# Optimization experiments

Measured on AMD Instinct MI355X. Metric: run time of the kernel, lower is better.

Reference implementation:

```python
import jax, jax.numpy as jnp
import numpy as np

HIDDEN = 2048
NUM_HEADS = 16
HEAD_DIM = HIDDEN // NUM_HEADS  # 128
ROPE_BASE = 10000.0
BATCH = 2
SEQ = 2048


def _rope_cos_sin(seq_len, dim, base):
    inv_freq = 1.0 / (base ** (jnp.arange(0, dim, 2, dtype=jnp.float32) / dim))
    t = jnp.arange(seq_len, dtype=jnp.float32)
    freqs = jnp.outer(t, inv_freq)              # [S, dim/2]
    emb = jnp.concatenate([freqs, freqs], -1)   # [S, dim]
    return jnp.cos(emb), jnp.sin(emb)


def _rotate_half(x):
    d = x.shape[-1] // 2
    return jnp.concatenate([-x[..., d:], x[..., :d]], axis=-1)


def setup_inputs() -> dict:
    key = jax.random.key(0)
    ks = jax.random.split(key, 5)
    s = 1.0 / np.sqrt(HIDDEN)
    return {
        "hidden_states": jax.random.normal(ks[0], (BATCH, SEQ, HIDDEN), jnp.float32),
        "wq": jax.random.normal(ks[1], (HIDDEN, HIDDEN), jnp.float32) * s,
        "wk": jax.random.normal(ks[2], (HIDDEN, HIDDEN), jnp.float32) * s,
        "wv": jax.random.normal(ks[3], (HIDDEN, HIDDEN), jnp.float32) * s,
        "wo": jax.random.normal(ks[4], (HIDDEN, HIDDEN), jnp.float32) * s,
    }


def reference(hidden_states, wq, wk, wv, wo):
    b, s, _ = hidden_states.shape
    # Linear(bias=False): y = x @ W.T
    def proj(x, w):
        y = jnp.einsum('bsh,dh->bsd', x, w)
        return y.reshape(b, s, NUM_HEADS, HEAD_DIM).transpose(0, 2, 1, 3)  # [B,H,S,D]

    q = proj(hidden_states, wq)
    k = proj(hidden_states, wk)
    v = proj(hidden_states, wv)

    cos, sin = _rope_cos_sin(s, HEAD_DIM, ROPE_BASE)  # [S, D], broadcasts over B,H
    q = q * cos + _rotate_half(q) * sin
    k = k * cos + _rotate_half(k) * sin

    scale = 1.0 / np.sqrt(HEAD_DIM)
    scores = jnp.einsum('bhqd,bhkd->bhqk', q, k) * scale          # [B,H,S,S]
    attn = jax.nn.softmax(scores.astype(jnp.float32), axis=-1).astype(q.dtype)
    out = jnp.einsum('bhqk,bhkd->bhqd', attn, v)                  # [B,H,S,D]
    out = out.transpose(0, 2, 1, 3).reshape(b, s, HIDDEN)
    return jnp.einsum('bsh,dh->bsd', out, wo)
```

## Files before the change

kernel.cpp:

```cpp
#include <hip/hip_runtime.h>
#include <cstdint>
#include <cstddef>

typedef unsigned short u16;
typedef __attribute__((ext_vector_type(8))) __bf16 bf16x8;
typedef __attribute__((ext_vector_type(4))) float f32x4;
typedef __attribute__((ext_vector_type(8))) u16 u16x8;

#define GAS __attribute__((address_space(1)))
#define LAS __attribute__((address_space(3)))

static __device__ __forceinline__ u16 f2bf(float f) {
  uint32_t u = __builtin_bit_cast(uint32_t, f);
  u += 0x7fffu + ((u >> 16) & 1u);
  return (u16)(u >> 16);
}
static __device__ __forceinline__ float bf2f(u16 v) {
  uint32_t u = ((uint32_t)v) << 16;
  return __builtin_bit_cast(float, u);
}
static __device__ __forceinline__ bf16x8 ldf(const u16* p) {
  return __builtin_bit_cast(bf16x8, *reinterpret_cast<const u16x8*>(p));
}
static __device__ __forceinline__ void gld16(const void* g, void* l) {
  __builtin_amdgcn_global_load_lds((GAS unsigned int*)(uintptr_t)g,
                                   (LAS unsigned int*)l, 16, 0, 0);
}

__global__ __launch_bounds__(256) void castk(const float* __restrict__ s,
                                             u16* __restrict__ d, int n4) {
  int i = blockIdx.x * 256 + threadIdx.x;
  if (i < n4) {
    const float4 v = reinterpret_cast<const float4*>(s)[i];
    ushort4 o;
    o.x = f2bf(v.x); o.y = f2bf(v.y); o.z = f2bf(v.z); o.w = f2bf(v.w);
    reinterpret_cast<ushort4*>(d)[i] = o;
  }
}

__global__ __launch_bounds__(256, 2)
void gemm_bt(const u16* __restrict__ A, const u16* __restrict__ B,
             void* __restrict__ Cp, int M, int N, int K, int out_f32) {
  __shared__ alignas(16) u16 smA[2][128 * 32];
  __shared__ alignas(16) u16 smB[2][128 * 32];
  const int tid  = threadIdx.x;
  const int lane = tid & 63;
  const int w    = tid >> 6;
  const long m0 = (long)blockIdx.y * 128;
  const long n0 = (long)blockIdx.x * 128;
  const int wm = (w >> 1) * 64, wn = (w & 1) * 64;

  f32x4 acc[4][4] = {};

  const int lin0 = w * 64 + lane;
  const int lin1 = (4 + w) * 64 + lane;
  const int lrow0 = lin0 >> 2, lcol0 = (lin0 & 3) * 8;
  const int lrow1 = lin1 >> 2, lcol1 = (lin1 & 3) * 8;

  auto stage = [&](int buf, int k0) {
    gld16(A + (m0 + lrow0) * K + k0 + lcol0, &smA[buf][(0 * 4 + w) * 512]);
    gld16(B + (n0 + lrow0) * K + k0 + lcol0, &smB[buf][(0 * 4 + w) * 512]);
    gld16(A + (m0 + lrow1) * K + k0 + lcol1, &smA[buf][(1 * 4 + w) * 512]);
    gld16(B + (n0 + lrow1) * K + k0 + lcol1, &smB[buf][(1 * 4 + w) * 512]);
  };
  auto compute = [&](int buf) {
    const u16* As = smA[buf];
    const u16* Bs = smB[buf];
    const int k8 = (lane >> 4) * 8;
    bf16x8 af[4], bfr[4];
#pragma unroll
    for (int t = 0; t < 4; ++t) {
      af[t]  = ldf(As + (wm + t * 16 + (lane & 15)) * 32 + k8);
      bfr[t] = ldf(Bs + (wn + t * 16 + (lane & 15)) * 32 + k8);
    }
#pragma unroll
    for (int i = 0; i < 4; ++i)
#pragma unroll
      for (int j = 0; j < 4; ++j)
        acc[i][j] = __builtin_amdgcn_mfma_f32_16x16x32_bf16(af[i], bfr[j], acc[i][j], 0, 0, 0);
  };

  stage(0, 0);
  __syncthreads();
  const int NT = K >> 5;
  for (int t = 0; t < NT; ++t) {
    if (t + 1 < NT) stage((t + 1) & 1, (t + 1) << 5);
    compute(t & 1);
    __syncthreads();
  }

#pragma unroll
  for (int i = 0; i < 4; ++i)
#pragma unroll
    for (int j = 0; j < 4; ++j)
#pragma unroll
      for (int r = 0; r < 4; ++r) {
        long row = m0 + wm + i * 16 + (lane >> 4) * 4 + r;
        long col = n0 + wn + j * 16 + (lane & 15);
        if (out_f32) ((float*)Cp)[row * N + col] = acc[i][j][r];
        else         ((u16*)Cp)[row * N + col]   = f2bf(acc[i][j][r]);
      }
}

__global__ __launch_bounds__(256) void rope_q(u16* __restrict__ Q) {
  const int m = blockIdx.x;
  const int pos = m & 2047;
  const int t = threadIdx.x;
  const int j = t & 63;
  const float invf = exp2f(-(float)j * 0.20762050593046014f);
  float sn, cs;
  sincosf((float)pos * invf, &sn, &cs);
  const float sc = 0.08838834764831845f;
#pragma unroll
  for (int h = t >> 6; h < 16; h += 4) {
    u16* p = Q + (size_t)m * 2048 + h * 128;
    float a = bf2f(p[j]), b = bf2f(p[j + 64]);
    p[j]      = f2bf((a * cs - b * sn) * sc);
    p[j + 64] = f2bf((b * cs + a * sn) * sc);
  }
}

__global__ __launch_bounds__(256) void rope_k(const u16* __restrict__ Kt, u16* __restrict__ Kb) {
  const int m = blockIdx.x;
  const int pos = m & 2047;
  const int bb = m >> 11;
  const int kb = pos >> 6;
  const int key = pos & 63;
  const int t = threadIdx.x;
  const int j = t & 63;
  const float invf = exp2f(-(float)j * 0.20762050593046014f);
  float sn, cs;
  sincosf((float)pos * invf, &sn, &cs);
  const int sw = (key & 7) << 3;
#pragma unroll
  for (int h = t >> 6; h < 16; h += 4) {
    const u16* p = Kt + (size_t)m * 2048 + h * 128;
    float a = bf2f(p[j]), b = bf2f(p[j + 64]);
    u16* dst = Kb + ((size_t)(bb * 16 + h) * 32 + kb) * 8192 + key * 128;
    dst[j ^ sw]        = f2bf(a * cs - b * sn);
    dst[(j + 64) ^ sw] = f2bf(b * cs + a * sn);
  }
}

__global__ __launch_bounds__(256) void transpose_v(const u16* __restrict__ Vt, u16* __restrict__ Vb) {
  __shared__ u16 sm[64][130];
  const int kb = blockIdx.x, bh = blockIdx.y;
  const int bb = bh >> 4, h = bh & 15;
  const int t = threadIdx.x;
#pragma unroll
  for (int r = 0; r < 4; ++r) {
    int c = r * 256 + t;
    int key = c >> 4, d0 = (c & 15) * 8;
    const u16* src = Vt + (size_t)(bb * 2048 + kb * 64 + key) * 2048 + h * 128 + d0;
    u16x8 v = *reinterpret_cast<const u16x8*>(src);
#pragma unroll
    for (int i = 0; i < 8; ++i) sm[key][d0 + i] = v[i];
  }
  __syncthreads();
  u16* dst = Vb + ((size_t)bh * 32 + kb) * 8192;
#pragma unroll
  for (int r = 0; r < 4; ++r) {
    int c = r * 256 + t;
    int key0 = (c & 7) * 8, d = c >> 3;
    u16x8 v;
#pragma unroll
    for (int i = 0; i < 8; ++i) v[i] = sm[key0 + i][d];
    *reinterpret_cast<u16x8*>(dst + d * 64 + (key0 ^ ((d & 7) << 3))) = v;
  }
}

__global__ __launch_bounds__(256, 2)
void flash_attn(const u16* __restrict__ Q, const u16* __restrict__ Kb,
                const u16* __restrict__ Vb, u16* __restrict__ O) {
  __shared__ alignas(16) u16 smK[64 * 128];
  __shared__ alignas(16) u16 smV[128 * 64];
  __shared__ alignas(16) u16 smP[4][16 * 64];

  const int f = blockIdx.x;
  const int bh = (f & 7) * 4 + (f >> 8);
  const int qb = (f >> 3) & 31;
  const int bb = bh >> 4, h = bh & 15;
  const int lane = threadIdx.x & 63, w = threadIdx.x >> 6;

  const int qrow = bb * 2048 + qb * 64 + w * 16 + (lane & 15);
  const u16* qp = Q + (size_t)qrow * 2048 + h * 128 + ((lane >> 4) * 8);
  bf16x8 qf[4];
#pragma unroll
  for (int kk = 0; kk < 4; ++kk) qf[kk] = ldf(qp + kk * 32);

  f32x4 oacc[8] = {};
  float mr[4] = {-__builtin_inff(), -__builtin_inff(), -__builtin_inff(), -__builtin_inff()};
  float lr[4] = {0.f, 0.f, 0.f, 0.f};

  const u16* kbase = Kb + (size_t)bh * 32 * 8192;
  const u16* vbase = Vb + (size_t)bh * 32 * 8192;

  for (int kb = 0; kb < 32; ++kb) {
    __syncthreads();
#pragma unroll
    for (int j = 0; j < 4; ++j) {
      int off = (j * 4 + w) * 512;
      gld16(kbase + (size_t)kb * 8192 + off + lane * 8, &smK[off]);
      gld16(vbase + (size_t)kb * 8192 + off + lane * 8, &smV[off]);
    }
    __syncthreads();

    f32x4 sacc[4] = {};
#pragma unroll
    for (int nt = 0; nt < 4; ++nt) {
      const int key = nt * 16 + (lane & 15);
      const int sw = (key & 7) << 3;
#pragma unroll
      for (int kk = 0; kk < 4; ++kk) {
        const int d = kk * 32 + (lane >> 4) * 8;
        bf16x8 kf = ldf(&smK[key * 128 + (d ^ sw)]);
        sacc[nt] = __builtin_amdgcn_mfma_f32_16x16x32_bf16(qf[kk], kf, sacc[nt], 0, 0, 0);
      }
    }

    float nm[4], fac[4];
#pragma unroll
    for (int r = 0; r < 4; ++r) {
      float mx = fmaxf(fmaxf(sacc[0][r], sacc[1][r]), fmaxf(sacc[2][r], sacc[3][r]));
#pragma unroll
      for (int o = 1; o < 16; o <<= 1) mx = fmaxf(mx, __shfl_xor(mx, o));
      nm[r] = fmaxf(mr[r], mx);
      fac[r] = exp2f((mr[r] - nm[r]) * 1.4426950408889634f);
      mr[r] = nm[r];
    }
#pragma unroll
    for (int nt = 0; nt < 4; ++nt)
#pragma unroll
      for (int r = 0; r < 4; ++r)
        sacc[nt][r] = exp2f((sacc[nt][r] - nm[r]) * 1.4426950408889634f);
#pragma unroll
    for (int r = 0; r < 4; ++r) {
      float s = (sacc[0][r] + sacc[1][r]) + (sacc[2][r] + sacc[3][r]);
#pragma unroll
      for (int o = 1; o < 16; o <<= 1) s += __shfl_xor(s, o);
      lr[r] = lr[r] * fac[r] + s;
    }
#pragma unroll
    for (int t = 0; t < 8; ++t)
#pragma unroll
      for (int r = 0; r < 4; ++r) oacc[t][r] *= fac[r];

    u16* pw = smP[w];
#pragma unroll
    for (int r = 0; r < 4; ++r) {
      const int row = (lane >> 4) * 4 + r;
      const int sw = (row & 7) << 3;
#pragma unroll
      for (int nt = 0; nt < 4; ++nt) {
        const int col = nt * 16 + (lane & 15);
        pw[row * 64 + (col ^ sw)] = f2bf(sacc[nt][r]);
      }
    }

#pragma unroll
    for (int kk2 = 0; kk2 < 2; ++kk2) {
      const int k0 = kk2 * 32 + (lane >> 4) * 8;
      const int prow = lane & 15;
      bf16x8 pf = ldf(&pw[prow * 64 + (k0 ^ ((prow & 7) << 3))]);
#pragma unroll
      for (int t = 0; t < 8; ++t) {
        const int d = t * 16 + (lane & 15);
        bf16x8 vf = ldf(&smV[d * 64 + (k0 ^ ((d & 7) << 3))]);
        oacc[t] = __builtin_amdgcn_mfma_f32_16x16x32_bf16(pf, vf, oacc[t], 0, 0, 0);
      }
    }
  }

#pragma unroll
  for (int r = 0; r < 4; ++r) lr[r] = 1.0f / lr[r];
  const int orow0 = bb * 2048 + qb * 64 + w * 16;
#pragma unroll
  for (int t = 0; t < 8; ++t)
#pragma unroll
    for (int r = 0; r < 4; ++r) {
      const int row = orow0 + (lane >> 4) * 4 + r;
      const int d = t * 16 + (lane & 15);
      O[(size_t)row * 2048 + h * 128 + d] = f2bf(oacc[t][r] * lr[r]);
    }
}

extern "C" void kernel_launch(void* const* d_in, const int* in_sizes, int n_in,
                              void* d_out, int out_size, void* d_ws, size_t ws_size,
                              hipStream_t stream) {
  const float* X  = (const float*)d_in[0];
  const float* Wq = (const float*)d_in[1];
  const float* Wk = (const float*)d_in[2];
  const float* Wv = (const float*)d_in[3];
  const float* Wo = (const float*)d_in[4];
  float* out = (float*)d_out;
  char* ws = (char*)d_ws;
  const size_t MB = 1u << 20;
  u16* Xb   = (u16*)(ws + 0   * MB);
  u16* Qb   = (u16*)(ws + 16  * MB);
  u16* Ktmp = (u16*)(ws + 32  * MB);
  u16* Vtmp = (u16*)(ws + 48  * MB);
  u16* Vblk = (u16*)(ws + 64  * MB);
  u16* Wqb  = (u16*)(ws + 80  * MB);
  u16* Wkb  = (u16*)(ws + 88  * MB);
  u16* Wvb  = (u16*)(ws + 96  * MB);
  u16* Wob  = (u16*)(ws + 104 * MB);
  u16* Kblk = Xb;
  u16* Ob   = Ktmp;

  castk<<<8192, 256, 0, stream>>>(X,  Xb,  2097152);
  castk<<<4096, 256, 0, stream>>>(Wq, Wqb, 1048576);
  castk<<<4096, 256, 0, stream>>>(Wk, Wkb, 1048576);
  castk<<<4096, 256, 0, stream>>>(Wv, Wvb, 1048576);
  castk<<<4096, 256, 0, stream>>>(Wo, Wob, 1048576);

  gemm_bt<<<dim3(16, 32), 256, 0, stream>>>(Xb, Wqb, Qb,   4096, 2048, 2048, 0);
  gemm_bt<<<dim3(16, 32), 256, 0, stream>>>(Xb, Wkb, Ktmp, 4096, 2048, 2048, 0);
  gemm_bt<<<dim3(16, 32), 256, 0, stream>>>(Xb, Wvb, Vtmp, 4096, 2048, 2048, 0);

  rope_q<<<4096, 256, 0, stream>>>(Qb);
  rope_k<<<4096, 256, 0, stream>>>(Ktmp, Kblk);
  transpose_v<<<dim3(32, 32), 256, 0, stream>>>(Vtmp, Vblk);

  flash_attn<<<1024, 256, 0, stream>>>(Qb, Kblk, Vblk, Ob);

  gemm_bt<<<dim3(16, 32), 256, 0, stream>>>(Ob, Wob, out, 4096, 2048, 2048, 1);
}
```

Measured before the change: 530.5 us.

## Fuse QKV projections into one 256x256-tile GEMM with pipelined LDS staging

The three Q/K/V projections become one GEMM over a concatenated weight, writing a row-interleaved QKV buffer. The old 128x128 GEMM is replaced by a 512-thread kernel with 256x256 tiles, K-step 64 split into halves, manual barriers and vmcnt waits, an XCD-aware block remap and s_setprio around MFMA bursts. Flash attention also raises wave priority around its MFMA loops. The aim is more data reuse per tile and fewer launches. The cost is that the output GEMM runs only 128 workgroups, which may underfill the GPU.

```diff
diff --git a/kernel.cpp b/kernel.cpp
--- a/kernel.cpp
+++ b/kernel.cpp
@@ -26,6 +26,7 @@
   __builtin_amdgcn_global_load_lds((GAS unsigned int*)(uintptr_t)g,
                                    (LAS unsigned int*)l, 16, 0, 0);
 }
+#define MFMA __builtin_amdgcn_mfma_f32_16x16x32_bf16
 
 __global__ __launch_bounds__(256) void castk(const float* __restrict__ s,
                                              u16* __restrict__ d, int n4) {
@@ -38,71 +39,139 @@
   }
 }
 
-__global__ __launch_bounds__(256, 2)
-void gemm_bt(const u16* __restrict__ A, const u16* __restrict__ B,
-             void* __restrict__ Cp, int M, int N, int K, int out_f32) {
-  __shared__ alignas(16) u16 smA[2][128 * 32];
-  __shared__ alignas(16) u16 smB[2][128 * 32];
-  const int tid  = threadIdx.x;
-  const int lane = tid & 63;
-  const int w    = tid >> 6;
-  const long m0 = (long)blockIdx.y * 128;
-  const long n0 = (long)blockIdx.x * 128;
-  const int wm = (w >> 1) * 64, wn = (w & 1) * 64;
-
-  f32x4 acc[4][4] = {};
-
-  const int lin0 = w * 64 + lane;
-  const int lin1 = (4 + w) * 64 + lane;
-  const int lrow0 = lin0 >> 2, lcol0 = (lin0 & 3) * 8;
-  const int lrow1 = lin1 >> 2, lcol1 = (lin1 & 3) * 8;
-
-  auto stage = [&](int buf, int k0) {
-    gld16(A + (m0 + lrow0) * K + k0 + lcol0, &smA[buf][(0 * 4 + w) * 512]);
-    gld16(B + (n0 + lrow0) * K + k0 + lcol0, &smB[buf][(0 * 4 + w) * 512]);
-    gld16(A + (m0 + lrow1) * K + k0 + lcol1, &smA[buf][(1 * 4 + w) * 512]);
-    gld16(B + (n0 + lrow1) * K + k0 + lcol1, &smB[buf][(1 * 4 + w) * 512]);
+__global__ __launch_bounds__(512, 2)
+void gemm256(const u16* __restrict__ A, const u16* __restrict__ B,
+             void* __restrict__ Cp, int M, int N, int K, int out_f32, int nbx) {
+  __shared__ alignas(16) u16 sm[8][8192];
+  const int tid = threadIdx.x;
+  const int lane = tid & 63, w = tid >> 6;
+  const int wm = w >> 2, wn = w & 3;
+  const int lo = lane & 15, hi8 = (lane >> 4) << 3;
+
+  const int nwg = gridDim.x;
+  const int id = blockIdx.x;
+  const int idp = (id & 7) * (nwg >> 3) + (id >> 3);
+  const long m0 = (long)(idp / nbx) * 256;
+  const long n0 = (long)(idp % nbx) * 256;
+
+  const int srow = w * 16 + (lane >> 2);
+  const int scol = (lane & 3) * 8;
+  const u16* pA0 = A + (size_t)(m0 + srow) * K + scol;
+  const u16* pA1 = A + (size_t)(m0 + 128 + srow) * K + scol;
+  const u16* pB0 = B + (size_t)(n0 + srow) * K + scol;
+  const u16* pB1 = B + (size_t)(n0 + 128 + srow) * K + scol;
+  const int ldso = w * 512;
+
+  auto stA = [&](int slot, int half, int k0) {
+    u16* d = sm[(slot << 2) | half];
+    gld16(pA0 + k0 + half * 32, d + ldso);
+    gld16(pA1 + k0 + half * 32, d + 4096 + ldso);
   };
-  auto compute = [&](int buf) {
-    const u16* As = smA[buf];
-    const u16* Bs = smB[buf];
-    const int k8 = (lane >> 4) * 8;
-    bf16x8 af[4], bfr[4];
-#pragma unroll
-    for (int t = 0; t < 4; ++t) {
-      af[t]  = ldf(As + (wm + t * 16 + (lane & 15)) * 32 + k8);
-      bfr[t] = ldf(Bs + (wn + t * 16 + (lane & 15)) * 32 + k8);
-    }
-#pragma unroll
-    for (int i = 0; i < 4; ++i)
-#pragma unroll
-      for (int j = 0; j < 4; ++j)
-        acc[i][j] = __builtin_amdgcn_mfma_f32_16x16x32_bf16(af[i], bfr[j], acc[i][j], 0, 0, 0);
+  auto stB = [&](int slot, int half, int k0) {
+    u16* d = sm[(slot << 2) | 2 | half];
+    gld16(pB0 + k0 + half * 32, d + ldso);
+    gld16(pB1 + k0 + half * 32, d + 4096 + ldso);
   };
 
-  stage(0, 0);
-  __syncthreads();
-  const int NT = K >> 5;
-  for (int t = 0; t < NT; ++t) {
-    if (t + 1 < NT) stage((t + 1) & 1, (t + 1) << 5);
-    compute(t & 1);
-    __syncthreads();
-  }
-
-#pragma unroll
-  for (int i = 0; i < 4; ++i)
-#pragma unroll
-    for (int j = 0; j < 4; ++j)
-#pragma unroll
-      for (int r = 0; r < 4; ++r) {
-        long row = m0 + wm + i * 16 + (lane >> 4) * 4 + r;
-        long col = n0 + wn + j * 16 + (lane & 15);
-        if (out_f32) ((float*)Cp)[row * N + col] = acc[i][j][r];
-        else         ((u16*)Cp)[row * N + col]   = f2bf(acc[i][j][r]);
+  const int aoff = (wm * 128 + lo) * 32 + hi8;
+  const int boff = (wn * 64 + lo) * 32 + hi8;
+
+  f32x4 acc[8][4] = {};
+
+  stA(0, 0, 0); stB(0, 0, 0); stA(0, 1, 0); stB(0, 1, 0);
+  asm volatile("s_waitcnt vmcnt(4)" ::: "memory");
+  __builtin_amdgcn_s_barrier();
+
+  const int NT = K >> 6;
+  for (int kt = 0; kt < NT; ++kt) {
+    const int s = kt & 1, so = s ^ 1;
+    const int kn = (kt + 1 < NT) ? ((kt + 1) << 6) : 0;
+    const u16* sA0 = sm[(s << 2) | 0];
+    const u16* sA1 = sm[(s << 2) | 1];
+    const u16* sB0 = sm[(s << 2) | 2];
+    const u16* sB1 = sm[(s << 2) | 3];
+
+    bf16x8 af[8], b0, b1;
+    b0 = ldf(sB0 + boff);
+    b1 = ldf(sB0 + boff + 512);
+#pragma unroll
+    for (int mf = 0; mf < 8; ++mf) af[mf] = ldf(sA0 + aoff + mf * 512);
+    stA(so, 0, kn);
+    __builtin_amdgcn_s_barrier();
+    asm volatile("s_waitcnt lgkmcnt(0)" ::: "memory");
+    __builtin_amdgcn_s_setprio(1);
+#pragma unroll
+    for (int mf = 0; mf < 8; ++mf) {
+      acc[mf][0] = MFMA(af[mf], b0, acc[mf][0], 0, 0, 0);
+      acc[mf][1] = MFMA(af[mf], b1, acc[mf][1], 0, 0, 0);
+    }
+    __builtin_amdgcn_s_setprio(0);
+    __builtin_amdgcn_s_barrier();
+    b0 = ldf(sB0 + boff + 1024);
+    b1 = ldf(sB0 + boff + 1536);
+    stB(so, 0, kn);
+    __builtin_amdgcn_s_barrier();
+    asm volatile("s_waitcnt lgkmcnt(0)" ::: "memory");
+    __builtin_amdgcn_s_setprio(1);
+#pragma unroll
+    for (int mf = 0; mf < 8; ++mf) {
+      acc[mf][2] = MFMA(af[mf], b0, acc[mf][2], 0, 0, 0);
+      acc[mf][3] = MFMA(af[mf], b1, acc[mf][3], 0, 0, 0);
+    }
+    __builtin_amdgcn_s_setprio(0);
+    asm volatile("s_waitcnt vmcnt(4)" ::: "memory");
+    __builtin_amdgcn_s_barrier();
+    b0 = ldf(sB1 + boff);
+    b1 = ldf(sB1 + boff + 512);
+#pragma unroll
+    for (int mf = 0; mf < 8; ++mf) af[mf] = ldf(sA1 + aoff + mf * 512);
+    stA(so, 1, kn);
+    __builtin_amdgcn_s_barrier();
+    asm volatile("s_waitcnt lgkmcnt(0)" ::: "memory");
+    __builtin_amdgcn_s_setprio(1);
+#pragma unroll
+    for (int mf = 0; mf < 8; ++mf) {
+      acc[mf][0] = MFMA(af[mf], b0, acc[mf][0], 0, 0, 0);
+      acc[mf][1] = MFMA(af[mf], b1, acc[mf][1], 0, 0, 0);
+    }
+    __builtin_amdgcn_s_setprio(0);
+    __builtin_amdgcn_s_barrier();
+    b0 = ldf(sB1 + boff + 1024);
+    b1 = ldf(sB1 + boff + 1536);
+    stB(so, 1, kn);
+    __builtin_amdgcn_s_barrier();
+    asm volatile("s_waitcnt lgkmcnt(0)" ::: "memory");
+    __builtin_amdgcn_s_setprio(1);
+#pragma unroll
+    for (int mf = 0; mf < 8; ++mf) {
+      acc[mf][2] = MFMA(af[mf], b0, acc[mf][2], 0, 0, 0);
+      acc[mf][3] = MFMA(af[mf], b1, acc[mf][3], 0, 0, 0);
+    }
+    __builtin_amdgcn_s_setprio(0);
+    asm volatile("s_waitcnt vmcnt(4)" ::: "memory");
+    __builtin_amdgcn_s_barrier();
+  }
+  asm volatile("s_waitcnt vmcnt(0)" ::: "memory");
+
+#pragma unroll
+  for (int mf = 0; mf < 8; ++mf)
+#pragma unroll
+    for (int nf = 0; nf < 4; ++nf) {
+      const long row = m0 + wm * 128 + mf * 16 + (lane >> 4) * 4;
+      const long col = n0 + wn * 64 + nf * 16 + lo;
+      if (out_f32) {
+        float* C = (float*)Cp;
+#pragma unroll
+        for (int r = 0; r < 4; ++r) C[(row + r) * N + col] = acc[mf][nf][r];
+      } else {
+        u16* C = (u16*)Cp;
+#pragma unroll
+        for (int r = 0; r < 4; ++r) C[(row + r) * N + col] = f2bf(acc[mf][nf][r]);
       }
-}
-
-__global__ __launch_bounds__(256) void rope_q(u16* __restrict__ Q) {
+    }
+}
+
+__global__ __launch_bounds__(256) void rope_q(u16* __restrict__ QKV) {
   const int m = blockIdx.x;
   const int pos = m & 2047;
   const int t = threadIdx.x;
@@ -113,14 +182,14 @@
   const float sc = 0.08838834764831845f;
 #pragma unroll
   for (int h = t >> 6; h < 16; h += 4) {
-    u16* p = Q + (size_t)m * 2048 + h * 128;
+    u16* p = QKV + (size_t)m * 6144 + h * 128;
     float a = bf2f(p[j]), b = bf2f(p[j + 64]);
     p[j]      = f2bf((a * cs - b * sn) * sc);
     p[j + 64] = f2bf((b * cs + a * sn) * sc);
   }
 }
 
-__global__ __launch_bounds__(256) void rope_k(const u16* __restrict__ Kt, u16* __restrict__ Kb) {
+__global__ __launch_bounds__(256) void rope_k(const u16* __restrict__ QKV, u16* __restrict__ Kb) {
   const int m = blockIdx.x;
   const int pos = m & 2047;
   const int bb = m >> 11;
@@ -134,7 +203,7 @@
   const int sw = (key & 7) << 3;
 #pragma unroll
   for (int h = t >> 6; h < 16; h += 4) {
-    const u16* p = Kt + (size_t)m * 2048 + h * 128;
+    const u16* p = QKV + (size_t)m * 6144 + 2048 + h * 128;
     float a = bf2f(p[j]), b = bf2f(p[j + 64]);
     u16* dst = Kb + ((size_t)(bb * 16 + h) * 32 + kb) * 8192 + key * 128;
     dst[j ^ sw]        = f2bf(a * cs - b * sn);
@@ -142,8 +211,8 @@
   }
 }
 
-__global__ __launch_bounds__(256) void transpose_v(const u16* __restrict__ Vt, u16* __restrict__ Vb) {
-  __shared__ u16 sm[64][130];
+__global__ __launch_bounds__(256) void transpose_v(const u16* __restrict__ QKV, u16* __restrict__ Vb) {
+  __shared__ u16 smv[64][130];
   const int kb = blockIdx.x, bh = blockIdx.y;
   const int bb = bh >> 4, h = bh & 15;
   const int t = threadIdx.x;
@@ -151,10 +220,10 @@
   for (int r = 0; r < 4; ++r) {
     int c = r * 256 + t;
     int key = c >> 4, d0 = (c & 15) * 8;
-    const u16* src = Vt + (size_t)(bb * 2048 + kb * 64 + key) * 2048 + h * 128 + d0;
+    const u16* src = QKV + (size_t)(bb * 2048 + kb * 64 + key) * 6144 + 4096 + h * 128 + d0;
     u16x8 v = *reinterpret_cast<const u16x8*>(src);
 #pragma unroll
-    for (int i = 0; i < 8; ++i) sm[key][d0 + i] = v[i];
+    for (int i = 0; i < 8; ++i) smv[key][d0 + i] = v[i];
   }
   __syncthreads();
   u16* dst = Vb + ((size_t)bh * 32 + kb) * 8192;
@@ -164,7 +233,7 @@
     int key0 = (c & 7) * 8, d = c >> 3;
     u16x8 v;
 #pragma unroll
-    for (int i = 0; i < 8; ++i) v[i] = sm[key0 + i][d];
+    for (int i = 0; i < 8; ++i) v[i] = smv[key0 + i][d];
     *reinterpret_cast<u16x8*>(dst + d * 64 + (key0 ^ ((d & 7) << 3))) = v;
   }
 }
@@ -183,7 +252,7 @@
   const int lane = threadIdx.x & 63, w = threadIdx.x >> 6;
 
   const int qrow = bb * 2048 + qb * 64 + w * 16 + (lane & 15);
-  const u16* qp = Q + (size_t)qrow * 2048 + h * 128 + ((lane >> 4) * 8);
+  const u16* qp = Q + (size_t)qrow * 6144 + h * 128 + ((lane >> 4) * 8);
   bf16x8 qf[4];
 #pragma unroll
   for (int kk = 0; kk < 4; ++kk) qf[kk] = ldf(qp + kk * 32);
@@ -206,6 +275,7 @@
     __syncthreads();
 
     f32x4 sacc[4] = {};
+    __builtin_amdgcn_s_setprio(1);
 #pragma unroll
     for (int nt = 0; nt < 4; ++nt) {
       const int key = nt * 16 + (lane & 15);
@@ -214,9 +284,10 @@
       for (int kk = 0; kk < 4; ++kk) {
         const int d = kk * 32 + (lane >> 4) * 8;
         bf16x8 kf = ldf(&smK[key * 128 + (d ^ sw)]);
-        sacc[nt] = __builtin_amdgcn_mfma_f32_16x16x32_bf16(qf[kk], kf, sacc[nt], 0, 0, 0);
+        sacc[nt] = MFMA(qf[kk], kf, sacc[nt], 0, 0, 0);
       }
     }
+    __builtin_amdgcn_s_setprio(0);
 
     float nm[4], fac[4];
 #pragma unroll
@@ -257,6 +328,7 @@
       }
     }
 
+    __builtin_amdgcn_s_setprio(1);
 #pragma unroll
     for (int kk2 = 0; kk2 < 2; ++kk2) {
       const int k0 = kk2 * 32 + (lane >> 4) * 8;
@@ -266,9 +338,10 @@
       for (int t = 0; t < 8; ++t) {
         const int d = t * 16 + (lane & 15);
         bf16x8 vf = ldf(&smV[d * 64 + (k0 ^ ((d & 7) << 3))]);
-        oacc[t] = __builtin_amdgcn_mfma_f32_16x16x32_bf16(pf, vf, oacc[t], 0, 0, 0);
+        oacc[t] = MFMA(pf, vf, oacc[t], 0, 0, 0);
       }
     }
+    __builtin_amdgcn_s_setprio(0);
   }
 
 #pragma unroll
@@ -295,33 +368,27 @@
   float* out = (float*)d_out;
   char* ws = (char*)d_ws;
   const size_t MB = 1u << 20;
-  u16* Xb   = (u16*)(ws + 0   * MB);
-  u16* Qb   = (u16*)(ws + 16  * MB);
-  u16* Ktmp = (u16*)(ws + 32  * MB);
-  u16* Vtmp = (u16*)(ws + 48  * MB);
-  u16* Vblk = (u16*)(ws + 64  * MB);
-  u16* Wqb  = (u16*)(ws + 80  * MB);
-  u16* Wkb  = (u16*)(ws + 88  * MB);
-  u16* Wvb  = (u16*)(ws + 96  * MB);
-  u16* Wob  = (u16*)(ws + 104 * MB);
-  u16* Kblk = Xb;
-  u16* Ob   = Ktmp;
-
-  castk<<<8192, 256, 0, stream>>>(X,  Xb,  2097152);
-  castk<<<4096, 256, 0, stream>>>(Wq, Wqb, 1048576);
-  castk<<<4096, 256, 0, stream>>>(Wk, Wkb, 1048576);
-  castk<<<4096, 256, 0, stream>>>(Wv, Wvb, 1048576);
+  u16* Xb    = (u16*)(ws + 0 * MB);
+  u16* QKVb  = (u16*)(ws + 16 * MB);
+  u16* Wqkvb = (u16*)(ws + 64 * MB);
+  u16* Wob   = (u16*)(ws + 96 * MB);
+  u16* Kblk  = Xb;
+  u16* Vblk  = (u16*)(ws + 64 * MB);
+  u16* Ob    = (u16*)(ws + 80 * MB);
+
+  castk<<<8192, 256, 0, stream>>>(X,  Xb, 2097152);
+  castk<<<4096, 256, 0, stream>>>(Wq, Wqkvb, 1048576);
+  castk<<<4096, 256, 0, stream>>>(Wk, Wqkvb + 4194304, 1048576);
+  castk<<<4096, 256, 0, stream>>>(Wv, Wqkvb + 8388608, 1048576);
   castk<<<4096, 256, 0, stream>>>(Wo, Wob, 1048576);
 
-  gemm_bt<<<dim3(16, 32), 256, 0, stream>>>(Xb, Wqb, Qb,   4096, 2048, 2048, 0);
-  gemm_bt<<<dim3(16, 32), 256, 0, stream>>>(Xb, Wkb, Ktmp, 4096, 2048, 2048, 0);
-  gemm_bt<<<dim3(16, 32), 256, 0, stream>>>(Xb, Wvb, Vtmp, 4096, 2048, 2048, 0);
-
-  rope_q<<<4096, 256, 0, stream>>>(Qb);
-  rope_k<<<4096, 256, 0, stream>>>(Ktmp, Kblk);
-  transpose_v<<<dim3(32, 32), 256, 0, stream>>>(Vtmp, Vblk);
-
-  flash_attn<<<1024, 256, 0, stream>>>(Qb, Kblk, Vblk, Ob);
-
-  gemm_bt<<<dim3(16, 32), 256, 0, stream>>>(Ob, Wob, out, 4096, 2048, 2048, 1);
-}
+  gemm256<<<384, 512, 0, stream>>>(Xb, Wqkvb, QKVb, 4096, 6144, 2048, 0, 24);
+
+  rope_q<<<4096, 256, 0, stream>>>(QKVb);
+  rope_k<<<4096, 256, 0, stream>>>(QKVb, Kblk);
+  transpose_v<<<dim3(32, 32), 256, 0, stream>>>(QKVb, Vblk);
+
+  flash_attn<<<1024, 256, 0, stream>>>(QKVb, Kblk, Vblk, Ob);
+
+  gemm256<<<128, 512, 0, stream>>>(Ob, Wob, out, 4096, 2048, 2048, 1, 8);
+}
```

New measurement: 499.7 us. -5.8%, faster.
